# Performance work log

Measured on AMD Instinct MI355X. Metric: run time of the kernel, lower is better.

## Reference

```python
import jax, jax.numpy as jnp
import numpy as np

B, T, D = 1024, 512, 128  # batch, history length, embedding = num_units


def setup_inputs() -> dict:
    key = jax.random.key(0)
    ks = jax.random.split(key, 5)
    s = 1.0 / np.sqrt(2 * D)
    return {
        "rnn_input": jax.random.normal(ks[0], (B, T, D), jnp.float32),
        "att_score": jax.random.uniform(ks[1], (B, T, 1), jnp.float32),
        "gate_kernel": jax.random.normal(ks[2], (2 * D, 2 * D), jnp.float32) * s,
        "gate_bias": jnp.ones((2 * D,), jnp.float32),  # TF GRUCell init: gate bias = 1.0
        "cand_kernel": jax.random.normal(ks[3], (2 * D, D), jnp.float32) * s,
        "cand_bias": jnp.zeros((D,), jnp.float32),
        "sequence_length": jax.random.randint(ks[4], (B, 1), 1, T + 1, jnp.int32),
    }


def reference(rnn_input, att_score, gate_kernel, gate_bias, cand_kernel, cand_bias, sequence_length):
    # AUGRU (VecAttGRUCell) dynamic_rnn, return_sequence=True
    Bv, Tv, Dv = rnn_input.shape
    lens = sequence_length.reshape(Bv)                      # tf.squeeze
    x_t = jnp.transpose(rnn_input, (1, 0, 2))               # [T,B,D]
    a_t = jnp.transpose(att_score, (1, 0, 2))               # [T,B,1]
    mask = (jnp.arange(Tv)[:, None] < lens[None, :])[..., None]  # [T,B,1] bool
    h0 = jnp.zeros((Bv, Dv), rnn_input.dtype)

    def step(h, xs):
        x, a, m = xs
        gi = jnp.concatenate([x, h], -1) @ gate_kernel + gate_bias
        r, u = jnp.split(jax.nn.sigmoid(gi), 2, axis=-1)
        c = jnp.tanh(jnp.concatenate([x, r * h], -1) @ cand_kernel + cand_bias)
        u = (1.0 - a) * u                                   # attention-gated update
        new_h = u * h + (1.0 - u) * c
        h_next = jnp.where(m, new_h, h)                     # state copy-through past length
        out = jnp.where(m, new_h, 0.0)                      # dynamic_rnn zeros past length
        return h_next, out

    _, outs = jax.lax.scan(step, h0, (x_t, a_t, mask))
    return jnp.transpose(outs, (1, 0, 2))                   # [B,T,D]
```

## Files before the change

### kernel.cpp

```cpp
#include <hip/hip_runtime.h>
#include <hip/hip_bf16.h>


#define Bn 1024
#define Tn 512
#define Dn 128

typedef __attribute__((ext_vector_type(8))) short short8;
typedef __attribute__((ext_vector_type(4))) short short4v;
typedef __attribute__((ext_vector_type(4))) float f32x4;

#define HS 132
#define BS 136

__device__ __forceinline__ short f2bf(float f) {
    __hip_bfloat16 h = __float2bfloat16(f);
    return __builtin_bit_cast(short, h);
}
__device__ __forceinline__ float sigmoidf_(float x) {
    float e = __expf(-x);
    return __builtin_amdgcn_rcpf(1.0f + e);
}
__device__ __forceinline__ float tanhf_(float x) {
    float e = __expf(-2.0f * x);
    return 2.0f * __builtin_amdgcn_rcpf(1.0f + e) - 1.0f;
}

__launch_bounds__(512, 2)
__global__ void augru_kernel(const float* __restrict__ X,
                             const float* __restrict__ ATT,
                             const float* __restrict__ GK,
                             const float* __restrict__ GB,
                             const float* __restrict__ CK,
                             const float* __restrict__ CB,
                             const int*   __restrict__ SL,
                             float* __restrict__ OUT) {
    __shared__ short hb [16 * BS];
    __shared__ short rhb[16 * BS];
    __shared__ short xb [2][16 * BS];
    __shared__ float hf [16 * HS];
    __shared__ float ub [16 * HS];
    __shared__ float abuf[2][16];
    __shared__ int   lenbuf[16];

    const int tid  = threadIdx.x;
    const int wid  = tid >> 6;
    const int lane = tid & 63;
    const int lm   = lane & 15;
    const int q    = lane >> 4;
    const int b0   = blockIdx.x * 16;

    short8 fgx[2][4], fgh[2][4], fcx[4], fch[4];
    const int gcolb = 32 * wid + lm;
    const int ccol  = 16 * wid + lm;
#pragma unroll
    for (int ns = 0; ns < 2; ++ns) {
        const int col = gcolb + 16 * ns;
#pragma unroll
        for (int ks = 0; ks < 4; ++ks) {
            short8 vx, vh;
#pragma unroll
            for (int j = 0; j < 8; ++j) {
                const int k = ks * 32 + q * 8 + j;
                vx[j] = f2bf(GK[k * 256 + col]);
                vh[j] = f2bf(GK[(128 + k) * 256 + col]);
            }
            fgx[ns][ks] = vx; fgh[ns][ks] = vh;
        }
    }
#pragma unroll
    for (int ks = 0; ks < 4; ++ks) {
        short8 vx, vh;
#pragma unroll
        for (int j = 0; j < 8; ++j) {
            const int k = ks * 32 + q * 8 + j;
            vx[j] = f2bf(CK[k * 128 + ccol]);
            vh[j] = f2bf(CK[(128 + k) * 128 + ccol]);
        }
        fcx[ks] = vx; fch[ks] = vh;
    }
    const float gb0 = GB[gcolb];
    const float gb1 = GB[gcolb + 16];
    const float cb  = CB[ccol];

    for (int i = tid; i < 16 * HS; i += 512) hf[i] = 0.0f;
    for (int i = tid; i < 16 * BS; i += 512) hb[i] = 0;
    if (tid < 16) {
        lenbuf[tid]  = SL[b0 + tid];
        abuf[0][tid] = ATT[(size_t)(b0 + tid) * Tn];
    }
    const int prow = tid >> 5;
    const int pcol = (tid & 31) * 4;
    {
        float4 v = *(const float4*)(X + ((size_t)(b0 + prow) * Tn + 0) * Dn + pcol);
        short4v s; s[0] = f2bf(v.x); s[1] = f2bf(v.y); s[2] = f2bf(v.z); s[3] = f2bf(v.w);
        *(short4v*)&xb[0][prow * BS + pcol] = s;
    }
    __syncthreads();

    int len_i[4];
#pragma unroll
    for (int i = 0; i < 4; ++i) len_i[i] = lenbuf[q * 4 + i];

    for (int t = 0; t < Tn; ++t) {
        const int cur = t & 1, nxt = cur ^ 1;

        const int tp = (t + 1 < Tn) ? t + 1 : Tn - 1;
        float4 xpre = *(const float4*)(X + ((size_t)(b0 + prow) * Tn + tp) * Dn + pcol);
        float  apre = (tid < 16) ? ATT[(size_t)(b0 + tid) * Tn + tp] : 0.0f;

        short8 ax[4], ah[4];
#pragma unroll
        for (int ks = 0; ks < 4; ++ks) {
            ax[ks] = *(const short8*)&xb[cur][lm * BS + ks * 32 + q * 8];
            ah[ks] = *(const short8*)&hb[lm * BS + ks * 32 + q * 8];
        }

        f32x4 g0 = {0.f, 0.f, 0.f, 0.f}, g1 = {0.f, 0.f, 0.f, 0.f};
#pragma unroll
        for (int ks = 0; ks < 4; ++ks) {
            g0 = __builtin_amdgcn_mfma_f32_16x16x32_bf16(ah[ks], fgh[0][ks], g0, 0, 0, 0);
            g1 = __builtin_amdgcn_mfma_f32_16x16x32_bf16(ah[ks], fgh[1][ks], g1, 0, 0, 0);
            g0 = __builtin_amdgcn_mfma_f32_16x16x32_bf16(ax[ks], fgx[0][ks], g0, 0, 0, 0);
            g1 = __builtin_amdgcn_mfma_f32_16x16x32_bf16(ax[ks], fgx[1][ks], g1, 0, 0, 0);
        }

        if (wid < 4) {
#pragma unroll
            for (int ns = 0; ns < 2; ++ns) {
                const int col = 32 * wid + 16 * ns + lm;
                const float bias = ns ? gb1 : gb0;
                const f32x4 gg = ns ? g1 : g0;
#pragma unroll
                for (int i = 0; i < 4; ++i) {
                    const int row = q * 4 + i;
                    const float r = sigmoidf_(gg[i] + bias);
                    rhb[row * BS + col] = f2bf(r * hf[row * HS + col]);
                }
            }
        } else {
#pragma unroll
            for (int ns = 0; ns < 2; ++ns) {
                const int cu = 32 * (wid - 4) + 16 * ns + lm;
                const float bias = ns ? gb1 : gb0;
                const f32x4 gg = ns ? g1 : g0;
#pragma unroll
                for (int i = 0; i < 4; ++i) {
                    const int row = q * 4 + i;
                    const float u = sigmoidf_(gg[i] + bias);
                    ub[row * HS + cu] = (1.0f - abuf[cur][row]) * u;
                }
            }
        }
        __syncthreads();

        f32x4 cc = {0.f, 0.f, 0.f, 0.f};
#pragma unroll
        for (int ks = 0; ks < 4; ++ks) {
            short8 arh = *(const short8*)&rhb[lm * BS + ks * 32 + q * 8];
            cc = __builtin_amdgcn_mfma_f32_16x16x32_bf16(arh, fch[ks], cc, 0, 0, 0);
            cc = __builtin_amdgcn_mfma_f32_16x16x32_bf16(ax[ks], fcx[ks], cc, 0, 0, 0);
        }

#pragma unroll
        for (int i = 0; i < 4; ++i) {
            const int row = q * 4 + i;
            const float cv   = tanhf_(cc[i] + cb);
            const float up   = ub[row * HS + ccol];
            const float hold = hf[row * HS + ccol];
            const float hn   = up * hold + (1.0f - up) * cv;
            const bool valid = (t < len_i[i]);
            const float hnext = valid ? hn : hold;
            OUT[((size_t)(b0 + row) * Tn + t) * Dn + ccol] = valid ? hn : 0.0f;
            hf[row * HS + ccol] = hnext;
            hb[row * BS + ccol] = f2bf(hnext);
        }

        {
            short4v s; s[0] = f2bf(xpre.x); s[1] = f2bf(xpre.y);
                       s[2] = f2bf(xpre.z); s[3] = f2bf(xpre.w);
            *(short4v*)&xb[nxt][prow * BS + pcol] = s;
            if (tid < 16) abuf[nxt][tid] = apre;
        }
        __syncthreads();
    }
}

extern "C" void kernel_launch(void* const* d_in, const int* in_sizes, int n_in,
                              void* d_out, int out_size, void* d_ws, size_t ws_size,
                              hipStream_t stream) {
    (void)in_sizes; (void)n_in; (void)d_ws; (void)ws_size; (void)out_size;
    const float* X   = (const float*)d_in[0];
    const float* ATT = (const float*)d_in[1];
    const float* GK  = (const float*)d_in[2];
    const float* GB  = (const float*)d_in[3];
    const float* CK  = (const float*)d_in[4];
    const float* CB  = (const float*)d_in[5];
    const int*   SL  = (const int*)d_in[6];
    float* OUT = (float*)d_out;

    augru_kernel<<<dim3(Bn / 16), dim3(512), 0, stream>>>(X, ATT, GK, GB, CK, CB, SL, OUT);
}
```

Baseline: 630.8 us.

## Remap gate columns so each wave owns r/u/c for same columns, keep h in registers

Each wave now computes the reset, update and candidate columns for the same 16 hidden units. That lets the fp32 hidden state and the update gate stay in registers, and the shared fp32 h and u buffers go away. The x-part of the candidate MFMA moves before the first barrier so it overlaps the gate work. Sigmoid and tanh are rewritten as exp2 with the bias pre-scaled by -log2(e). Per-step shared-memory traffic falls and the work is balanced across waves, at the cost of more weight-fragment registers per wave (24 short8 instead of 24 split differently), which could add register pressure.

```diff
diff --git a/kernel.cpp b/kernel.cpp
--- a/kernel.cpp
+++ b/kernel.cpp
@@ -10,21 +10,15 @@
 typedef __attribute__((ext_vector_type(4))) short short4v;
 typedef __attribute__((ext_vector_type(4))) float f32x4;
 
-#define HS 132
 #define BS 136
+#define NLOG2E (-1.4426950408889634f)
 
 __device__ __forceinline__ short f2bf(float f) {
     __hip_bfloat16 h = __float2bfloat16(f);
     return __builtin_bit_cast(short, h);
 }
-__device__ __forceinline__ float sigmoidf_(float x) {
-    float e = __expf(-x);
-    return __builtin_amdgcn_rcpf(1.0f + e);
-}
-__device__ __forceinline__ float tanhf_(float x) {
-    float e = __expf(-2.0f * x);
-    return 2.0f * __builtin_amdgcn_rcpf(1.0f + e) - 1.0f;
-}
+
+#define MFMA(a, b, c) __builtin_amdgcn_mfma_f32_16x16x32_bf16((a), (b), (c), 0, 0, 0)
 
 __launch_bounds__(512, 2)
 __global__ void augru_kernel(const float* __restrict__ X,
@@ -38,8 +32,6 @@
     __shared__ short hb [16 * BS];
     __shared__ short rhb[16 * BS];
     __shared__ short xb [2][16 * BS];
-    __shared__ float hf [16 * HS];
-    __shared__ float ub [16 * HS];
     __shared__ float abuf[2][16];
     __shared__ int   lenbuf[16];
 
@@ -49,41 +41,29 @@
     const int lm   = lane & 15;
     const int q    = lane >> 4;
     const int b0   = blockIdx.x * 16;
+    const int ccol = 16 * wid + lm;
 
-    short8 fgx[2][4], fgh[2][4], fcx[4], fch[4];
-    const int gcolb = 32 * wid + lm;
-    const int ccol  = 16 * wid + lm;
-#pragma unroll
-    for (int ns = 0; ns < 2; ++ns) {
-        const int col = gcolb + 16 * ns;
-#pragma unroll
-        for (int ks = 0; ks < 4; ++ks) {
-            short8 vx, vh;
-#pragma unroll
-            for (int j = 0; j < 8; ++j) {
-                const int k = ks * 32 + q * 8 + j;
-                vx[j] = f2bf(GK[k * 256 + col]);
-                vh[j] = f2bf(GK[(128 + k) * 256 + col]);
-            }
-            fgx[ns][ks] = vx; fgh[ns][ks] = vh;
-        }
-    }
+    short8 fgx0[4], fgx1[4], fgh0[4], fgh1[4], fcx[4], fch[4];
 #pragma unroll
     for (int ks = 0; ks < 4; ++ks) {
-        short8 vx, vh;
+        short8 v0, v1, v2, v3, v4, v5;
 #pragma unroll
         for (int j = 0; j < 8; ++j) {
             const int k = ks * 32 + q * 8 + j;
-            vx[j] = f2bf(CK[k * 128 + ccol]);
-            vh[j] = f2bf(CK[(128 + k) * 128 + ccol]);
+            v0[j] = f2bf(GK[k * 256 + ccol]);
+            v1[j] = f2bf(GK[k * 256 + 128 + ccol]);
+            v2[j] = f2bf(GK[(128 + k) * 256 + ccol]);
+            v3[j] = f2bf(GK[(128 + k) * 256 + 128 + ccol]);
+            v4[j] = f2bf(CK[k * 128 + ccol]);
+            v5[j] = f2bf(CK[(128 + k) * 128 + ccol]);
         }
-        fcx[ks] = vx; fch[ks] = vh;
+        fgx0[ks] = v0; fgx1[ks] = v1; fgh0[ks] = v2; fgh1[ks] = v3;
+        fcx[ks] = v4;  fch[ks] = v5;
     }
-    const float gb0 = GB[gcolb];
-    const float gb1 = GB[gcolb + 16];
-    const float cb  = CB[ccol];
+    const float bp0 = GB[ccol] * NLOG2E;
+    const float bp1 = GB[128 + ccol] * NLOG2E;
+    const float cbp = CB[ccol] * (2.0f * NLOG2E);
 
-    for (int i = tid; i < 16 * HS; i += 512) hf[i] = 0.0f;
     for (int i = tid; i < 16 * BS; i += 512) hb[i] = 0;
     if (tid < 16) {
         lenbuf[tid]  = SL[b0 + tid];
@@ -92,13 +72,14 @@
     const int prow = tid >> 5;
     const int pcol = (tid & 31) * 4;
     {
-        float4 v = *(const float4*)(X + ((size_t)(b0 + prow) * Tn + 0) * Dn + pcol);
+        float4 v = *(const float4*)(X + ((size_t)(b0 + prow) * Tn) * Dn + pcol);
         short4v s; s[0] = f2bf(v.x); s[1] = f2bf(v.y); s[2] = f2bf(v.z); s[3] = f2bf(v.w);
         *(short4v*)&xb[0][prow * BS + pcol] = s;
     }
     __syncthreads();
 
     int len_i[4];
+    float h_reg[4] = {0.f, 0.f, 0.f, 0.f};
 #pragma unroll
     for (int i = 0; i < 4; ++i) len_i[i] = lenbuf[q * 4 + i];
 
@@ -109,6 +90,10 @@
         float4 xpre = *(const float4*)(X + ((size_t)(b0 + prow) * Tn + tp) * Dn + pcol);
         float  apre = (tid < 16) ? ATT[(size_t)(b0 + tid) * Tn + tp] : 0.0f;
 
+        float am[4];
+#pragma unroll
+        for (int i = 0; i < 4; ++i) am[i] = 1.0f - abuf[cur][q * 4 + i];
+
         short8 ax[4], ah[4];
 #pragma unroll
         for (int ks = 0; ks < 4; ++ks) {
@@ -116,64 +101,44 @@
             ah[ks] = *(const short8*)&hb[lm * BS + ks * 32 + q * 8];
         }
 
-        f32x4 g0 = {0.f, 0.f, 0.f, 0.f}, g1 = {0.f, 0.f, 0.f, 0.f};
+        f32x4 g0 = {0.f,0.f,0.f,0.f}, g1 = {0.f,0.f,0.f,0.f}, cc = {0.f,0.f,0.f,0.f};
 #pragma unroll
         for (int ks = 0; ks < 4; ++ks) {
-            g0 = __builtin_amdgcn_mfma_f32_16x16x32_bf16(ah[ks], fgh[0][ks], g0, 0, 0, 0);
-            g1 = __builtin_amdgcn_mfma_f32_16x16x32_bf16(ah[ks], fgh[1][ks], g1, 0, 0, 0);
-            g0 = __builtin_amdgcn_mfma_f32_16x16x32_bf16(ax[ks], fgx[0][ks], g0, 0, 0, 0);
-            g1 = __builtin_amdgcn_mfma_f32_16x16x32_bf16(ax[ks], fgx[1][ks], g1, 0, 0, 0);
+            g0 = MFMA(ah[ks], fgh0[ks], g0);
+            g1 = MFMA(ah[ks], fgh1[ks], g1);
+            g0 = MFMA(ax[ks], fgx0[ks], g0);
+            g1 = MFMA(ax[ks], fgx1[ks], g1);
+            cc = MFMA(ax[ks], fcx[ks], cc);
         }
 
-        if (wid < 4) {
+        float up[4];
 #pragma unroll
-            for (int ns = 0; ns < 2; ++ns) {
-                const int col = 32 * wid + 16 * ns + lm;
-                const float bias = ns ? gb1 : gb0;
-                const f32x4 gg = ns ? g1 : g0;
-#pragma unroll
-                for (int i = 0; i < 4; ++i) {
-                    const int row = q * 4 + i;
-                    const float r = sigmoidf_(gg[i] + bias);
-                    rhb[row * BS + col] = f2bf(r * hf[row * HS + col]);
-                }
-            }
-        } else {
-#pragma unroll
-            for (int ns = 0; ns < 2; ++ns) {
-                const int cu = 32 * (wid - 4) + 16 * ns + lm;
-                const float bias = ns ? gb1 : gb0;
-                const f32x4 gg = ns ? g1 : g0;
-#pragma unroll
-                for (int i = 0; i < 4; ++i) {
-                    const int row = q * 4 + i;
-                    const float u = sigmoidf_(gg[i] + bias);
-                    ub[row * HS + cu] = (1.0f - abuf[cur][row]) * u;
-                }
-            }
+        for (int i = 0; i < 4; ++i) {
+            const int row = q * 4 + i;
+            const float er = __builtin_amdgcn_exp2f(fmaf(g0[i], NLOG2E, bp0));
+            const float r  = __builtin_amdgcn_rcpf(1.0f + er);
+            rhb[row * BS + ccol] = f2bf(r * h_reg[i]);
+            const float eu = __builtin_amdgcn_exp2f(fmaf(g1[i], NLOG2E, bp1));
+            up[i] = am[i] * __builtin_amdgcn_rcpf(1.0f + eu);
         }
         __syncthreads();
 
-        f32x4 cc = {0.f, 0.f, 0.f, 0.f};
 #pragma unroll
         for (int ks = 0; ks < 4; ++ks) {
             short8 arh = *(const short8*)&rhb[lm * BS + ks * 32 + q * 8];
-            cc = __builtin_amdgcn_mfma_f32_16x16x32_bf16(arh, fch[ks], cc, 0, 0, 0);
-            cc = __builtin_amdgcn_mfma_f32_16x16x32_bf16(ax[ks], fcx[ks], cc, 0, 0, 0);
+            cc = MFMA(arh, fch[ks], cc);
         }
 
 #pragma unroll
         for (int i = 0; i < 4; ++i) {
             const int row = q * 4 + i;
-            const float cv   = tanhf_(cc[i] + cb);
-            const float up   = ub[row * HS + ccol];
-            const float hold = hf[row * HS + ccol];
-            const float hn   = up * hold + (1.0f - up) * cv;
+            const float e  = __builtin_amdgcn_exp2f(fmaf(cc[i], 2.0f * NLOG2E, cbp));
+            const float cv = fmaf(2.0f, __builtin_amdgcn_rcpf(1.0f + e), -1.0f);
+            const float hn = fmaf(up[i], h_reg[i] - cv, cv);
             const bool valid = (t < len_i[i]);
-            const float hnext = valid ? hn : hold;
+            h_reg[i] = valid ? hn : h_reg[i];
             OUT[((size_t)(b0 + row) * Tn + t) * Dn + ccol] = valid ? hn : 0.0f;
-            hf[row * HS + ccol] = hnext;
-            hb[row * BS + ccol] = f2bf(hnext);
+            hb[row * BS + ccol] = f2bf(h_reg[i]);
         }
 
         {
```

New measurement: 749.9 us. 18.9% more time.
